# Kernel optimization log

Measured on AMD Instinct MI355X. Metric: run time of the kernel, lower is better.

Reference implementation:

```python
import jax, jax.numpy as jnp
import numpy as np

EMBED_DIM = 128


def setup_inputs() -> dict:
    key = jax.random.key(0)
    k = jax.random.split(key, 6)
    B, S, H, D = 4, 512, 768, EMBED_DIM
    ent_embeddings = jax.random.normal(k[0], (B, S, H), jnp.float32)
    ent_type_ids = jax.random.randint(k[1], (B, S), 0, 10)  # entity-type labels (>=0)
    ent_mask = jax.random.randint(k[2], (B, S), 0, 2)       # 0/1 attention mask
    W_mu = jax.random.normal(k[3], (H, D), jnp.float32) / np.sqrt(H)
    b_mu = jnp.zeros((D,), jnp.float32)
    W_sigma = jax.random.normal(k[4], (H, D), jnp.float32) / np.sqrt(H)
    b_sigma = jnp.zeros((D,), jnp.float32)
    return dict(ent_embeddings=ent_embeddings, ent_type_ids=ent_type_ids, ent_mask=ent_mask,
                W_mu=W_mu, b_mu=b_mu, W_sigma=W_sigma, b_sigma=b_sigma)


def _pairwise_kl(mu, sigma, dim):
    # Symmetrized KL between diagonal Gaussians for all pairs (i=row, j=col).
    # Decomposed into rank-D contractions instead of materializing [N,N,D].
    inv = 1.0 / sigma                               # [N,D]
    S_log = jnp.sum(jnp.log(sigma), axis=1)         # [N] sum_d log sigma (1e-14 inside log is negligible in fp32)
    A = jnp.einsum('id,jd->ij', inv, sigma)         # sum_d sigma_j/sigma_i
    q = jnp.sum(mu * mu * inv, axis=1)              # [N] sum_d mu_i^2/sigma_i
    cross = jnp.einsum('id,jd->ij', mu * inv, mu)   # sum_d mu_i*mu_j/sigma_i
    quad = jnp.einsum('id,jd->ij', inv, mu * mu)    # sum_d mu_j^2/sigma_i
    md_i = q[:, None] - 2.0 * cross + quad          # sum_d (mu_i-mu_j)^2 / sigma_i
    ld = S_log[None, :] - S_log[:, None]            # sum_d log(sigma_j/sigma_i)
    ij_kl = 0.5 * (A + md_i - dim - ld)
    ji_kl = 0.5 * (A.T + md_i.T - dim + ld)
    return 0.5 * (ij_kl + ji_kl)


def reference(ent_embeddings, ent_type_ids, ent_mask, W_mu, b_mu, W_sigma, b_sigma):
    D = EMBED_DIM
    h = jax.nn.relu(ent_embeddings)                 # dropout in eval mode (identity)
    mu = (h @ W_mu + b_mu).reshape(-1, D)           # [N,D]
    sigma = (jax.nn.elu(h @ W_sigma + b_sigma) + 1.0 + 1e-14).reshape(-1, D)

    labels = ent_type_ids.reshape(-1)
    valid = (ent_mask.reshape(-1) == 1) & (labels >= 0)   # consider_mutual_O=True: no labels>0 filter

    # loss_mask: ALL coordinates of mu differ (kills diagonal / duplicate rows)
    alldiff = jnp.all(mu[:, None, :] != mu[None, :, :], axis=-1)  # [N,N]
    pair_valid = valid[:, None] & valid[None, :]
    lab_eq = labels[:, None] == labels[None, :]
    denom_m = (alldiff & pair_valid).astype(mu.dtype)             # loss_mask
    num_w = (lab_eq & alldiff & pair_valid).astype(mu.dtype)      # loss_weights

    loss = -_pairwise_kl(mu, sigma, D)              # loss_type='KL'

    # NT-Xent, temperature=1
    e = jnp.exp(loss)
    cnts = jnp.sum(num_w, axis=1)
    loss_num = jnp.sum(e * num_w, axis=1)
    loss_den = jnp.sum(e * denom_m, axis=1)
    sel = cnts > 0
    safe = lambda v: jnp.where(sel, v, 1.0)
    lf = -jnp.log2(safe(loss_num)) + jnp.log2(safe(loss_den)) + jnp.log2(safe(cnts))
    n_sel = jnp.maximum(jnp.sum(sel.astype(mu.dtype)), 1.0)
    return jnp.sum(jnp.where(sel, lf, 0.0)) / n_sel
```

## Files before the change

kernel.cpp:

```cpp
#include <hip/hip_runtime.h>
#include <math.h>

#define NROWS 2048
#define HDIM 768
#define DDIM 128
#define FEAT 512
#define DCAP 2048
#define TSLOTS 8192

typedef __attribute__((ext_vector_type(8))) short bf16x8;
typedef __attribute__((ext_vector_type(4))) float f32x4;

__device__ __forceinline__ void mergeState(float& m, float& n, float& d,
                                           float m2, float n2, float d2) {
  float M = fmaxf(m, m2);
  float s1 = (m >= M) ? 1.0f : __expf(m - M);
  float s2 = (m2 >= M) ? 1.0f : __expf(m2 - M);
  n = n * s1 + n2 * s2;
  d = d * s1 + d2 * s2;
  m = M;
}

__device__ __forceinline__ unsigned short bfhi(float x) {
  unsigned int u = __float_as_uint(x);
  return (unsigned short)((u + 0x7fffu + ((u >> 16) & 1u)) >> 16);
}

__device__ __forceinline__ void gload16(const void* g, void* l) {
  __builtin_amdgcn_global_load_lds(
      (const __attribute__((address_space(1))) void*)g,
      (__attribute__((address_space(3))) void*)l, 16, 0, 0);
}

__global__ __launch_bounds__(256) void k0_prep(
    const float* __restrict__ E, const float* __restrict__ Wmu,
    const float* __restrict__ Wsg,
    unsigned short* __restrict__ Ehi, unsigned short* __restrict__ Wthi,
    unsigned long long* __restrict__ tab, int* __restrict__ rowflag,
    int* __restrict__ dupcnt)
{
  const int bid = blockIdx.x, t = threadIdx.x;
  if (bid < 768) {
    const int base = bid * 2048 + t * 8;
    float4 v0 = *reinterpret_cast<const float4*>(E + base);
    float4 v1 = *reinterpret_cast<const float4*>(E + base + 4);
    const float v[8] = {v0.x, v0.y, v0.z, v0.w, v1.x, v1.y, v1.z, v1.w};
    unsigned short h[8];
    #pragma unroll
    for (int i = 0; i < 8; ++i) h[i] = bfhi(fmaxf(v[i], 0.f));
    *reinterpret_cast<ushort4*>(Ehi + base)     = make_ushort4(h[0], h[1], h[2], h[3]);
    *reinterpret_cast<ushort4*>(Ehi + base + 4) = make_ushort4(h[4], h[5], h[6], h[7]);
  } else if (bid < 864) {
    const int tid = (bid - 768) * 256 + t;
    const int c = tid / 96, kc = (tid % 96) * 8;
    unsigned short h[8];
    #pragma unroll
    for (int j = 0; j < 8; ++j) {
      float w = (c < 128) ? Wmu[(size_t)(kc + j) * DDIM + c]
                          : Wsg[(size_t)(kc + j) * DDIM + (c - 128)];
      h[j] = bfhi(w);
    }
    const size_t o = (size_t)c * HDIM + kc;
    *reinterpret_cast<ushort4*>(Wthi + o)     = make_ushort4(h[0], h[1], h[2], h[3]);
    *reinterpret_cast<ushort4*>(Wthi + o + 4) = make_ushort4(h[4], h[5], h[6], h[7]);
  } else if (bid < 872) {
    const int i4 = (bid - 864) * 1024 + t * 4;
    #pragma unroll
    for (int k = 0; k < 4; ++k) tab[i4 + k] = 0ULL;
    rowflag[(bid - 864) * 256 + t] = 0;
  } else {
    if (t == 0) dupcnt[0] = 0;
  }
}

__global__ __launch_bounds__(256) void k1m(
    const unsigned short* __restrict__ Ehi,
    const unsigned short* __restrict__ Wthi,
    float* __restrict__ Cpart)
{
  __shared__ unsigned short lds[12288];
  const int t = threadIdx.x;
  const int bid = blockIdx.x;
  const int mt = bid & 31, nt = (bid >> 5) & 1, ks = bid >> 6;
  const int i0 = mt * 64, n0 = nt * 128, kbase = ks * 192;

  const unsigned short* gF[3];
  size_t goff[3];
  int lpb[3];
  #pragma unroll
  for (int rr = 0; rr < 3; ++rr) {
    if (rr == 0) {
      const int s = t, gq = s >> 6, row = s & 63;
      gF[0] = Ehi;
      goff[0] = (size_t)(i0 + row) * HDIM + kbase + gq * 8;
      lpb[0] = (t & ~63) * 8;
    } else {
      const int s = (rr - 1) * 256 + t, gq = s >> 7, row = s & 127;
      gF[rr] = Wthi;
      goff[rr] = (size_t)(n0 + row) * HDIM + kbase + gq * 8;
      lpb[rr] = 2048 + (s & ~63) * 8;
    }
  }

  f32x4 acc[2][4];
  #pragma unroll
  for (int a = 0; a < 2; ++a)
    #pragma unroll
    for (int b = 0; b < 4; ++b) {
      acc[a][b][0] = 0.f; acc[a][b][1] = 0.f; acc[a][b][2] = 0.f; acc[a][b][3] = 0.f;
    }

  const int wid = t >> 6, lane = t & 63;
  const int wr = wid >> 1, wc = wid & 1;
  const int gq = lane >> 4, c0 = lane & 15;

  auto stage = [&](int it, int buf) {
    unsigned short* lb = lds + buf * 6144;
    #pragma unroll
    for (int rr = 0; rr < 3; ++rr)
      gload16(gF[rr] + goff[rr] + it * 32, lb + lpb[rr]);
  };

  stage(0, 0);
  __syncthreads();

  for (int it = 0; it < 6; ++it) {
    if (it < 5) {
      stage(it + 1, (it + 1) & 1);
      asm volatile("s_waitcnt vmcnt(3)" ::: "memory");
    } else {
      asm volatile("s_waitcnt vmcnt(0)" ::: "memory");
    }
    __builtin_amdgcn_s_barrier();
    {
      const unsigned short* lb = lds + (it & 1) * 6144;
      bf16x8 ah[2], bh[4];
      #pragma unroll
      for (int fa = 0; fa < 2; ++fa) {
        const int ia = gq * 512 + (wr * 32 + fa * 16 + c0) * 8;
        ah[fa] = *reinterpret_cast<const bf16x8*>(lb + ia);
      }
      #pragma unroll
      for (int fb = 0; fb < 4; ++fb) {
        const int ib = 2048 + gq * 1024 + (wc * 64 + fb * 16 + c0) * 8;
        bh[fb] = *reinterpret_cast<const bf16x8*>(lb + ib);
      }
      #pragma unroll
      for (int fa = 0; fa < 2; ++fa)
        #pragma unroll
        for (int fb = 0; fb < 4; ++fb)
          acc[fa][fb] = __builtin_amdgcn_mfma_f32_16x16x32_bf16(
              ah[fa], bh[fb], acc[fa][fb], 0, 0, 0);
    }
    __builtin_amdgcn_s_barrier();
  }

  #pragma unroll
  for (int fa = 0; fa < 2; ++fa)
    #pragma unroll
    for (int fb = 0; fb < 4; ++fb)
      #pragma unroll
      for (int r = 0; r < 4; ++r) {
        const int row = i0 + wr * 32 + fa * 16 + gq * 4 + r;
        const int col = n0 + wc * 64 + fb * 16 + c0;
        Cpart[((size_t)ks * NROWS + row) * 256 + col] = acc[fa][fb][r];
      }
}

__global__ __launch_bounds__(256) void k1e(
    const float* __restrict__ Cpart, const float* __restrict__ bmu,
    const float* __restrict__ bsg,
    unsigned short* __restrict__ Ftl,
    float* __restrict__ qout, unsigned long long* __restrict__ tab,
    int* __restrict__ rowflag, int* __restrict__ dupcnt,
    int2* __restrict__ duplist)
{
  __shared__ unsigned short fbuf[16][520];
  const int t = threadIdx.x;
  const int row16 = t >> 4, cw = t & 15, c8 = cw * 8;
  const int g = blockIdx.x;
  const int rg = g * 16 + row16;

  float vm[8], vs[8];
  #pragma unroll
  for (int j = 0; j < 8; ++j) { vm[j] = 0.f; vs[j] = 0.f; }
  #pragma unroll
  for (int ks = 0; ks < 4; ++ks) {
    const float* src = &Cpart[((size_t)ks * NROWS + rg) * 256];
    float4 m0 = *reinterpret_cast<const float4*>(src + c8);
    float4 m1 = *reinterpret_cast<const float4*>(src + c8 + 4);
    float4 s0 = *reinterpret_cast<const float4*>(src + 128 + c8);
    float4 s1 = *reinterpret_cast<const float4*>(src + 128 + c8 + 4);
    vm[0] += m0.x; vm[1] += m0.y; vm[2] += m0.z; vm[3] += m0.w;
    vm[4] += m1.x; vm[5] += m1.y; vm[6] += m1.z; vm[7] += m1.w;
    vs[0] += s0.x; vs[1] += s0.y; vs[2] += s0.z; vs[3] += s0.w;
    vs[4] += s1.x; vs[5] += s1.y; vs[6] += s1.z; vs[7] += s1.w;
  }

  float q = 0.f;
  unsigned int hx = 0u, hs2 = 0u;
  unsigned short o1[8], o2[8], o3[8], o4[8];
  #pragma unroll
  for (int j = 0; j < 8; ++j) {
    const int col = c8 + j;
    float z = vs[j] + bsg[col];
    float s = (z > 0.f ? z + 1.0f : __expf(z)) + 1e-14f;
    float mu = vm[j] + bmu[col];
    float inv = 1.0f / s;
    o1[j] = bfhi(inv);
    o2[j] = bfhi(s + mu * mu);
    o3[j] = bfhi(-2.0f * mu * inv);
    o4[j] = bfhi(mu);
    q += mu * mu * inv;
    unsigned int b = __float_as_uint(mu);
    if (b == 0x80000000u) b = 0u;
    unsigned int hm = (b ^ ((unsigned int)col * 0x9E3779B9u)) * 0x85EBCA6Bu;
    hm ^= hm >> 13;
    hx ^= hm;
    hs2 += hm * 0xC2B2AE35u;
  }
  *reinterpret_cast<ushort4*>(&fbuf[row16][      c8])     = make_ushort4(o1[0], o1[1], o1[2], o1[3]);
  *reinterpret_cast<ushort4*>(&fbuf[row16][      c8 + 4]) = make_ushort4(o1[4], o1[5], o1[6], o1[7]);
  *reinterpret_cast<ushort4*>(&fbuf[row16][128 + c8])     = make_ushort4(o2[0], o2[1], o2[2], o2[3]);
  *reinterpret_cast<ushort4*>(&fbuf[row16][128 + c8 + 4]) = make_ushort4(o2[4], o2[5], o2[6], o2[7]);
  *reinterpret_cast<ushort4*>(&fbuf[row16][256 + c8])     = make_ushort4(o3[0], o3[1], o3[2], o3[3]);
  *reinterpret_cast<ushort4*>(&fbuf[row16][256 + c8 + 4]) = make_ushort4(o3[4], o3[5], o3[6], o3[7]);
  *reinterpret_cast<ushort4*>(&fbuf[row16][384 + c8])     = make_ushort4(o4[0], o4[1], o4[2], o4[3]);
  *reinterpret_cast<ushort4*>(&fbuf[row16][384 + c8 + 4]) = make_ushort4(o4[4], o4[5], o4[6], o4[7]);

  #pragma unroll
  for (int o = 8; o; o >>= 1) q += __shfl_xor(q, o, 16);
  #pragma unroll
  for (int o = 1; o < 16; o <<= 1) {
    hx  ^= (unsigned int)__shfl_xor((int)hx, o, 16);
    hs2 += (unsigned int)__shfl_xor((int)hs2, o, 16);
  }
  if (cw == 0) {
    qout[rg] = q;
    unsigned long long key = (((unsigned long long)hx << 32) | hs2) & ~0xFFFULL;
    if (key == 0ULL) key = 0x123456789000ULL;
    const unsigned long long me = key | (unsigned long long)(rg + 1);
    unsigned int h = (hx ^ (hs2 * 0x9E3779B9u)) & (TSLOTS - 1);
    for (;;) {
      unsigned long long old = atomicCAS(&tab[h], 0ULL, me);
      if (old == 0ULL) break;
      if ((old & ~0xFFFULL) == key) {
        int r2 = (int)(old & 0xFFFULL) - 1;
        rowflag[rg] = 1; rowflag[r2] = 1;
        int e = atomicAdd(dupcnt, 1);
        if (e < DCAP) duplist[e] = make_int2(min(rg, r2), max(rg, r2));
      }
      h = (h + 1u) & (TSLOTS - 1);
    }
  }
  __syncthreads();

  #pragma unroll
  for (int u = 0; u < 4; ++u) {
    const int f = u * 256 + t;
    const int kb = f >> 6, ln = f & 63;
    const int gq2 = ln >> 4, cc = ln & 15;
    uint4 v = *reinterpret_cast<const uint4*>(&fbuf[cc][kb * 32 + gq2 * 8]);
    *reinterpret_cast<uint4*>(&Ftl[((size_t)(g * 16 + kb)) * 512 + ln * 8]) = v;
  }
}

__global__ __launch_bounds__(1024, 4) void k2_mfma(
    const unsigned short* __restrict__ Ftl,
    const float* __restrict__ qv, const int* __restrict__ labels,
    const int* __restrict__ msk, const int* __restrict__ rowflag,
    const int* __restrict__ dupcnt, const int2* __restrict__ duplist,
    float4* __restrict__ ipart)
{
  __shared__ unsigned short Blds[65536];
  const int t = threadIdx.x;
  const int orig = blockIdx.x;
  const int xcd = orig & 7, idx = orig >> 3;
  const int bi = (xcd >> 1) * 4 + (idx >> 3);
  const int bj = (xcd & 1) * 8 + (idx & 7);
  const int i0 = bi * 128, j0 = bj * 128;
  const int wid = t >> 6, lane = t & 63;
  const int wr = wid >> 2, wc = wid & 3;
  const int gq = lane >> 4, c0 = lane & 15;

  {
    const unsigned short* Bsrc = Ftl + (size_t)bj * 65536;
    #pragma unroll
    for (int u = 0; u < 8; ++u) {
      const int slot = u * 1024 + t;
      uint4 v = *reinterpret_cast<const uint4*>(Bsrc + slot * 8);
      *reinterpret_cast<uint4*>(Blds + slot * 8) = v;
    }
  }
  __syncthreads();

  const int ga0 = bi * 8 + wr * 2;
  const unsigned short* fl = Ftl + lane * 8;
  const unsigned short* bl = Blds + lane * 8;
  const int hb0 = wc * 2;

  f32x4 acc[2][2];
  #pragma unroll
  for (int a = 0; a < 2; ++a)
    #pragma unroll
    for (int b = 0; b < 2; ++b) {
      acc[a][b][0] = 0.f; acc[a][b][1] = 0.f; acc[a][b][2] = 0.f; acc[a][b][3] = 0.f;
    }

  bf16x8 Abuf[3][2];

#define LOADA(kb_, s_)                                                         \
  {                                                                            \
    Abuf[s_][0] = *reinterpret_cast<const bf16x8*>(fl + ((ga0    ) * 16 + (kb_)) * 512); \
    Abuf[s_][1] = *reinterpret_cast<const bf16x8*>(fl + ((ga0 + 1) * 16 + (kb_)) * 512); \
  }

#define STEP(kb_, s_)                                                          \
  {                                                                            \
    const int kbb_ = (kb_) ^ 4;                                                \
    bf16x8 B0 = *reinterpret_cast<const bf16x8*>(bl + ((hb0    ) * 16 + kbb_) * 512); \
    bf16x8 B1 = *reinterpret_cast<const bf16x8*>(bl + ((hb0 + 1) * 16 + kbb_) * 512); \
    acc[0][0] = __builtin_amdgcn_mfma_f32_16x16x32_bf16(Abuf[s_][0], B0, acc[0][0], 0, 0, 0); \
    acc[0][1] = __builtin_amdgcn_mfma_f32_16x16x32_bf16(Abuf[s_][0], B1, acc[0][1], 0, 0, 0); \
    acc[1][0] = __builtin_amdgcn_mfma_f32_16x16x32_bf16(Abuf[s_][1], B0, acc[1][0], 0, 0, 0); \
    acc[1][1] = __builtin_amdgcn_mfma_f32_16x16x32_bf16(Abuf[s_][1], B1, acc[1][1], 0, 0, 0); \
  }

  LOADA(0, 0);
  LOADA(1, 1);
  #pragma unroll
  for (int kb = 0; kb < 16; ++kb) {
    if (kb < 14) { LOADA(kb + 2, (kb + 2) % 3); }
    STEP(kb, kb % 3);
  }
#undef LOADA
#undef STEP

  const int ndup = min(dupcnt[0], DCAP);
  int ljv[2]; float qjv[2]; int fjv[2]; int gjv[2];
  #pragma unroll
  for (int fb = 0; fb < 2; ++fb) {
    const int gj = j0 + wc * 32 + fb * 16 + c0;
    const int lab = labels[gj];
    ljv[fb] = (msk[gj] == 1 && lab >= 0) ? lab : -1;
    qjv[fb] = qv[gj];
    fjv[fb] = rowflag[gj];
    gjv[fb] = gj;
  }
  #pragma unroll
  for (int fa = 0; fa < 2; ++fa) {
    const int ibase = i0 + wr * 32 + fa * 16 + gq * 4;
    int li4[4], mi4[4], fi4[4]; float qi4[4];
    *reinterpret_cast<int4*>(li4)   = *reinterpret_cast<const int4*>(labels + ibase);
    *reinterpret_cast<int4*>(mi4)   = *reinterpret_cast<const int4*>(msk + ibase);
    *reinterpret_cast<int4*>(fi4)   = *reinterpret_cast<const int4*>(rowflag + ibase);
    *reinterpret_cast<float4*>(qi4) = *reinterpret_cast<const float4*>(qv + ibase);
    #pragma unroll
    for (int r = 0; r < 4; ++r) {
      const int gi = ibase + r;
      const int li = (mi4[r] == 1 && li4[r] >= 0) ? li4[r] : -1;
      float m = -INFINITY, n = 0.f, d = 0.f, c = 0.f;
      if (li >= 0) {
        #pragma unroll
        for (int fb = 0; fb < 2; ++fb) {
          const int lj = ljv[fb];
          bool inc = (lj >= 0) && (gi != gjv[fb]);
          if (inc && fi4[r] && fjv[fb]) {
            int plo = min(gi, gjv[fb]), phi = max(gi, gjv[fb]);
            for (int e = 0; e < ndup; ++e) {
              int2 p = duplist[e];
              if (p.x == plo && p.y == phi) { inc = false; break; }
            }
          }
          if (inc) {
            float S = acc[fa][fb][r];
            float l = 64.0f - 0.25f * (qi4[r] + qjv[fb] + S);
            float w = (li == lj) ? 1.0f : 0.0f;
            mergeState(m, n, d, l, w, 1.0f);
            c += w;
          }
        }
      }
      #pragma unroll
      for (int o = 1; o < 16; o <<= 1) {
        float m2 = __shfl_xor(m, o);
        float n2 = __shfl_xor(n, o);
        float d2 = __shfl_xor(d, o);
        float c2 = __shfl_xor(c, o);
        mergeState(m, n, d, m2, n2, d2);
        c += c2;
      }
      if (c0 == 0)
        ipart[(size_t)(bj * 4 + wc) * NROWS + gi] = make_float4(m, n, d, c);
    }
  }
}

__global__ __launch_bounds__(256) void k3a(const float4* __restrict__ ipart,
                                           float2* __restrict__ bsums)
{
  const int r = blockIdx.x * 256 + threadIdx.x;
  float m = -INFINITY, n = 0.f, d = 0.f, c = 0.f;
  #pragma unroll 8
  for (int js = 0; js < 64; ++js) {
    float4 p = ipart[(size_t)js * NROWS + r];
    mergeState(m, n, d, p.x, p.y, p.z);
    c += p.w;
  }
  float lf = 0.f, ns = 0.f;
  if (c > 0.f) {
    lf = log2f(d) - log2f(n) + log2f(c);
    ns = 1.f;
  }
  #pragma unroll
  for (int o = 32; o; o >>= 1) {
    lf += __shfl_down(lf, o);
    ns += __shfl_down(ns, o);
  }
  __shared__ float sl[4], sn[4];
  const int wid = threadIdx.x >> 6;
  if ((threadIdx.x & 63) == 0) { sl[wid] = lf; sn[wid] = ns; }
  __syncthreads();
  if (threadIdx.x == 0)
    bsums[blockIdx.x] = make_float2(sl[0] + sl[1] + sl[2] + sl[3],
                                    sn[0] + sn[1] + sn[2] + sn[3]);
}

__global__ __launch_bounds__(64) void k3b(const float2* __restrict__ bsums,
                                          float* __restrict__ out)
{
  if (threadIdx.x == 0) {
    float L = 0.f, C = 0.f;
    for (int b = 0; b < 8; ++b) { L += bsums[b].x; C += bsums[b].y; }
    out[0] = L / fmaxf(C, 1.0f);
  }
}

extern "C" void kernel_launch(void* const* d_in, const int* in_sizes, int n_in,
                              void* d_out, int out_size, void* d_ws, size_t ws_size,
                              hipStream_t stream) {
  const float* E   = (const float*)d_in[0];
  const int*   tid = (const int*)d_in[1];
  const int*   msk = (const int*)d_in[2];
  const float* Wmu = (const float*)d_in[3];
  const float* bmu = (const float*)d_in[4];
  const float* Wsg = (const float*)d_in[5];
  const float* bsg = (const float*)d_in[6];

  unsigned char* w = (unsigned char*)d_ws;
  unsigned short* Ehi  = (unsigned short*)w;  w += (size_t)NROWS * HDIM * 2;
  unsigned short* Wthi = (unsigned short*)w;  w += (size_t)256 * HDIM * 2;
  unsigned short* Ftl  = (unsigned short*)w;  w += (size_t)NROWS * FEAT * 2;
  float* Cpart         = (float*)w;           w += (size_t)4 * NROWS * 256 * 4;
  float* qv            = (float*)w;           w += (size_t)NROWS * 4;
  unsigned long long* tab = (unsigned long long*)w; w += (size_t)TSLOTS * 8;
  int* rowflag         = (int*)w;             w += (size_t)NROWS * 4;
  int* dupcnt          = (int*)w;             w += 256;
  float2* bsums        = (float2*)w;          w += 256;
  int2* duplist        = (int2*)w;            w += (size_t)DCAP * 8;
  float4* ipart        = (float4*)w;          w += (size_t)64 * NROWS * 16;

  k0_prep<<<873, 256, 0, stream>>>(E, Wmu, Wsg, Ehi, Wthi,
                                   tab, rowflag, dupcnt);
  k1m<<<256, 256, 0, stream>>>(Ehi, Wthi, Cpart);
  k1e<<<128, 256, 0, stream>>>(Cpart, bmu, bsg, Ftl, qv,
                               tab, rowflag, dupcnt, duplist);
  k2_mfma<<<256, 1024, 0, stream>>>(Ftl, qv, tid, msk, rowflag,
                                    dupcnt, duplist, ipart);
  k3a<<<8, 256, 0, stream>>>(ipart, bsums);
  k3b<<<1, 64, 0, stream>>>(bsums, (float*)d_out);
}
```

Baseline: 48.14 us.

## Fuse bf16 conversion prep into GEMM kernel and merge final reduction kernels

Removes the separate prep kernel by having the projection GEMM read fp32 embeddings and weights directly, apply relu and bf16 rounding in registers, and write to LDS through a register-staged double buffer. It also folds the workspace zeroing into the GEMM kernel. The two final reduction kernels are merged using atomics plus a last-block ticket. This removes two launches and the bf16 intermediate round trip, at the cost of strided scalar weight loads and losing async global-to-LDS loads.

```diff
diff --git a/kernel.cpp b/kernel.cpp
--- a/kernel.cpp
+++ b/kernel.cpp
@@ -26,81 +26,62 @@
   return (unsigned short)((u + 0x7fffu + ((u >> 16) & 1u)) >> 16);
 }
 
-__device__ __forceinline__ void gload16(const void* g, void* l) {
-  __builtin_amdgcn_global_load_lds(
-      (const __attribute__((address_space(1))) void*)g,
-      (__attribute__((address_space(3))) void*)l, 16, 0, 0);
-}
-
-__global__ __launch_bounds__(256) void k0_prep(
+__global__ __launch_bounds__(256) void k1m(
     const float* __restrict__ E, const float* __restrict__ Wmu,
-    const float* __restrict__ Wsg,
-    unsigned short* __restrict__ Ehi, unsigned short* __restrict__ Wthi,
+    const float* __restrict__ Wsg, float* __restrict__ Cpart,
     unsigned long long* __restrict__ tab, int* __restrict__ rowflag,
-    int* __restrict__ dupcnt)
-{
-  const int bid = blockIdx.x, t = threadIdx.x;
-  if (bid < 768) {
-    const int base = bid * 2048 + t * 8;
-    float4 v0 = *reinterpret_cast<const float4*>(E + base);
-    float4 v1 = *reinterpret_cast<const float4*>(E + base + 4);
-    const float v[8] = {v0.x, v0.y, v0.z, v0.w, v1.x, v1.y, v1.z, v1.w};
-    unsigned short h[8];
-    #pragma unroll
-    for (int i = 0; i < 8; ++i) h[i] = bfhi(fmaxf(v[i], 0.f));
-    *reinterpret_cast<ushort4*>(Ehi + base)     = make_ushort4(h[0], h[1], h[2], h[3]);
-    *reinterpret_cast<ushort4*>(Ehi + base + 4) = make_ushort4(h[4], h[5], h[6], h[7]);
-  } else if (bid < 864) {
-    const int tid = (bid - 768) * 256 + t;
-    const int c = tid / 96, kc = (tid % 96) * 8;
-    unsigned short h[8];
-    #pragma unroll
-    for (int j = 0; j < 8; ++j) {
-      float w = (c < 128) ? Wmu[(size_t)(kc + j) * DDIM + c]
-                          : Wsg[(size_t)(kc + j) * DDIM + (c - 128)];
-      h[j] = bfhi(w);
-    }
-    const size_t o = (size_t)c * HDIM + kc;
-    *reinterpret_cast<ushort4*>(Wthi + o)     = make_ushort4(h[0], h[1], h[2], h[3]);
-    *reinterpret_cast<ushort4*>(Wthi + o + 4) = make_ushort4(h[4], h[5], h[6], h[7]);
-  } else if (bid < 872) {
-    const int i4 = (bid - 864) * 1024 + t * 4;
-    #pragma unroll
-    for (int k = 0; k < 4; ++k) tab[i4 + k] = 0ULL;
-    rowflag[(bid - 864) * 256 + t] = 0;
-  } else {
-    if (t == 0) dupcnt[0] = 0;
-  }
-}
-
-__global__ __launch_bounds__(256) void k1m(
-    const unsigned short* __restrict__ Ehi,
-    const unsigned short* __restrict__ Wthi,
-    float* __restrict__ Cpart)
+    int* __restrict__ dupcnt, float* __restrict__ gsum)
 {
   __shared__ unsigned short lds[12288];
   const int t = threadIdx.x;
   const int bid = blockIdx.x;
+
+  if (t < 32) tab[bid * 32 + t] = 0ULL;
+  if (t < 8)  rowflag[bid * 8 + t] = 0;
+  if (bid == 0 && t == 0) {
+    dupcnt[0] = 0;
+    gsum[0] = 0.f; gsum[1] = 0.f; gsum[2] = 0.f;
+  }
+
   const int mt = bid & 31, nt = (bid >> 5) & 1, ks = bid >> 6;
-  const int i0 = mt * 64, n0 = nt * 128, kbase = ks * 192;
-
-  const unsigned short* gF[3];
-  size_t goff[3];
-  int lpb[3];
-  #pragma unroll
-  for (int rr = 0; rr < 3; ++rr) {
-    if (rr == 0) {
-      const int s = t, gq = s >> 6, row = s & 63;
-      gF[0] = Ehi;
-      goff[0] = (size_t)(i0 + row) * HDIM + kbase + gq * 8;
-      lpb[0] = (t & ~63) * 8;
-    } else {
-      const int s = (rr - 1) * 256 + t, gq = s >> 7, row = s & 127;
-      gF[rr] = Wthi;
-      goff[rr] = (size_t)(n0 + row) * HDIM + kbase + gq * 8;
-      lpb[rr] = 2048 + (s & ~63) * 8;
-    }
-  }
+  const int i0 = mt * 64, kbase = ks * 192;
+  const float* Wsrc = nt ? Wsg : Wmu;
+
+  const int akg = t & 3, arow = t >> 2;
+  const int bcol = t & 127, bkh = t >> 7;
+  const int aw  = akg * 512 + arow * 8;
+  const int bw0 = 2048 + (bkh * 2) * 1024 + bcol * 8;
+  const int bw1 = bw0 + 1024;
+
+  float4 rA0, rA1; float rB[16];
+
+  auto loadRegs = [&](int it) {
+    const int ka = kbase + it * 32;
+    const float* ep = E + (size_t)(i0 + arow) * HDIM + ka + akg * 8;
+    rA0 = *reinterpret_cast<const float4*>(ep);
+    rA1 = *reinterpret_cast<const float4*>(ep + 4);
+    const float* wp = Wsrc + (size_t)(ka + bkh * 16) * DDIM + bcol;
+    #pragma unroll
+    for (int j = 0; j < 16; ++j) rB[j] = wp[(size_t)j * DDIM];
+  };
+
+  auto writeLds = [&](int buf) {
+    unsigned short* lb = lds + buf * 6144;
+    unsigned short ha[8];
+    ha[0] = bfhi(fmaxf(rA0.x, 0.f)); ha[1] = bfhi(fmaxf(rA0.y, 0.f));
+    ha[2] = bfhi(fmaxf(rA0.z, 0.f)); ha[3] = bfhi(fmaxf(rA0.w, 0.f));
+    ha[4] = bfhi(fmaxf(rA1.x, 0.f)); ha[5] = bfhi(fmaxf(rA1.y, 0.f));
+    ha[6] = bfhi(fmaxf(rA1.z, 0.f)); ha[7] = bfhi(fmaxf(rA1.w, 0.f));
+    *reinterpret_cast<ushort4*>(lb + aw)     = make_ushort4(ha[0], ha[1], ha[2], ha[3]);
+    *reinterpret_cast<ushort4*>(lb + aw + 4) = make_ushort4(ha[4], ha[5], ha[6], ha[7]);
+    unsigned short hb[16];
+    #pragma unroll
+    for (int j = 0; j < 16; ++j) hb[j] = bfhi(rB[j]);
+    *reinterpret_cast<ushort4*>(lb + bw0)     = make_ushort4(hb[0],  hb[1],  hb[2],  hb[3]);
+    *reinterpret_cast<ushort4*>(lb + bw0 + 4) = make_ushort4(hb[4],  hb[5],  hb[6],  hb[7]);
+    *reinterpret_cast<ushort4*>(lb + bw1)     = make_ushort4(hb[8],  hb[9],  hb[10], hb[11]);
+    *reinterpret_cast<ushort4*>(lb + bw1 + 4) = make_ushort4(hb[12], hb[13], hb[14], hb[15]);
+  };
 
   f32x4 acc[2][4];
   #pragma unroll
@@ -114,24 +95,12 @@
   const int wr = wid >> 1, wc = wid & 1;
   const int gq = lane >> 4, c0 = lane & 15;
 
-  auto stage = [&](int it, int buf) {
-    unsigned short* lb = lds + buf * 6144;
-    #pragma unroll
-    for (int rr = 0; rr < 3; ++rr)
-      gload16(gF[rr] + goff[rr] + it * 32, lb + lpb[rr]);
-  };
-
-  stage(0, 0);
+  loadRegs(0);
+  writeLds(0);
+  loadRegs(1);
   __syncthreads();
 
   for (int it = 0; it < 6; ++it) {
-    if (it < 5) {
-      stage(it + 1, (it + 1) & 1);
-      asm volatile("s_waitcnt vmcnt(3)" ::: "memory");
-    } else {
-      asm volatile("s_waitcnt vmcnt(0)" ::: "memory");
-    }
-    __builtin_amdgcn_s_barrier();
     {
       const unsigned short* lb = lds + (it & 1) * 6144;
       bf16x8 ah[2], bh[4];
@@ -152,9 +121,14 @@
           acc[fa][fb] = __builtin_amdgcn_mfma_f32_16x16x32_bf16(
               ah[fa], bh[fb], acc[fa][fb], 0, 0, 0);
     }
-    __builtin_amdgcn_s_barrier();
-  }
-
+    if (it < 5) {
+      writeLds((it + 1) & 1);
+      if (it < 4) loadRegs(it + 2);
+    }
+    __syncthreads();
+  }
+
+  const int n0 = nt * 128;
   #pragma unroll
   for (int fa = 0; fa < 2; ++fa)
     #pragma unroll
@@ -396,8 +370,9 @@
   }
 }
 
-__global__ __launch_bounds__(256) void k3a(const float4* __restrict__ ipart,
-                                           float2* __restrict__ bsums)
+__global__ __launch_bounds__(256) void k3(const float4* __restrict__ ipart,
+                                          float* __restrict__ gsum,
+                                          float* __restrict__ out)
 {
   const int r = blockIdx.x * 256 + threadIdx.x;
   float m = -INFINITY, n = 0.f, d = 0.f, c = 0.f;
@@ -421,18 +396,18 @@
   const int wid = threadIdx.x >> 6;
   if ((threadIdx.x & 63) == 0) { sl[wid] = lf; sn[wid] = ns; }
   __syncthreads();
-  if (threadIdx.x == 0)
-    bsums[blockIdx.x] = make_float2(sl[0] + sl[1] + sl[2] + sl[3],
-                                    sn[0] + sn[1] + sn[2] + sn[3]);
-}
-
-__global__ __launch_bounds__(64) void k3b(const float2* __restrict__ bsums,
-                                          float* __restrict__ out)
-{
   if (threadIdx.x == 0) {
-    float L = 0.f, C = 0.f;
-    for (int b = 0; b < 8; ++b) { L += bsums[b].x; C += bsums[b].y; }
-    out[0] = L / fmaxf(C, 1.0f);
+    float L = sl[0] + sl[1] + sl[2] + sl[3];
+    float C = sn[0] + sn[1] + sn[2] + sn[3];
+    atomicAdd(&gsum[0], L);
+    atomicAdd(&gsum[1], C);
+    __threadfence();
+    unsigned int tk = atomicAdd(reinterpret_cast<unsigned int*>(gsum + 2), 1u);
+    if (tk == 7u) {
+      float Lt = atomicAdd(&gsum[0], 0.f);
+      float Ct = atomicAdd(&gsum[1], 0.f);
+      out[0] = Lt / fmaxf(Ct, 1.0f);
+    }
   }
 }
 
@@ -448,25 +423,20 @@
   const float* bsg = (const float*)d_in[6];
 
   unsigned char* w = (unsigned char*)d_ws;
-  unsigned short* Ehi  = (unsigned short*)w;  w += (size_t)NROWS * HDIM * 2;
-  unsigned short* Wthi = (unsigned short*)w;  w += (size_t)256 * HDIM * 2;
   unsigned short* Ftl  = (unsigned short*)w;  w += (size_t)NROWS * FEAT * 2;
   float* Cpart         = (float*)w;           w += (size_t)4 * NROWS * 256 * 4;
   float* qv            = (float*)w;           w += (size_t)NROWS * 4;
   unsigned long long* tab = (unsigned long long*)w; w += (size_t)TSLOTS * 8;
   int* rowflag         = (int*)w;             w += (size_t)NROWS * 4;
   int* dupcnt          = (int*)w;             w += 256;
-  float2* bsums        = (float2*)w;          w += 256;
+  float* gsum          = (float*)w;           w += 256;
   int2* duplist        = (int2*)w;            w += (size_t)DCAP * 8;
   float4* ipart        = (float4*)w;          w += (size_t)64 * NROWS * 16;
 
-  k0_prep<<<873, 256, 0, stream>>>(E, Wmu, Wsg, Ehi, Wthi,
-                                   tab, rowflag, dupcnt);
-  k1m<<<256, 256, 0, stream>>>(Ehi, Wthi, Cpart);
+  k1m<<<256, 256, 0, stream>>>(E, Wmu, Wsg, Cpart, tab, rowflag, dupcnt, gsum);
   k1e<<<128, 256, 0, stream>>>(Cpart, bmu, bsg, Ftl, qv,
                                tab, rowflag, dupcnt, duplist);
   k2_mfma<<<256, 1024, 0, stream>>>(Ftl, qv, tid, msk, rowflag,
                                     dupcnt, duplist, ipart);
-  k3a<<<8, 256, 0, stream>>>(ipart, bsums);
-  k3b<<<1, 64, 0, stream>>>(bsums, (float*)d_out);
-}
+  k3<<<8, 256, 0, stream>>>(ipart, gsum, (float*)d_out);
+}
```

Measured after the change: 45.25 us, median of 2. -6.0%, faster.
